# Performance work log

Hardware: AMD Instinct MI355X
Metric: run time of the kernel (lower is better)

## Reference

```python
import jax, jax.numpy as jnp
import numpy as np

VOCAB = 30000  # opts.numofingr
EPS = 1e-12


def setup_inputs() -> dict:
    key = jax.random.key(0)
    ks = jax.random.split(key, 8)
    B, L = 4096, 20
    ingrs = jax.random.randint(ks[0], (B, L), 0, VOCAB, dtype=jnp.int32)
    lengths = jax.random.randint(ks[1], (B,), 0, 21, dtype=jnp.int32)
    # MLP params: Linear(VOCAB,512) -> ReLU -> Linear(512,1024) -> ReLU -> Linear(1024,2047)
    # Stored so that one-hot @ W1 == W1[ingr]; i.e. W1 has shape [VOCAB, 512].
    W1 = jax.random.normal(ks[2], (VOCAB, 512), dtype=jnp.float32) * (1.0 / np.sqrt(VOCAB))
    b1 = jax.random.normal(ks[3], (512,), dtype=jnp.float32) * 0.01
    W2 = jax.random.normal(ks[4], (512, 1024), dtype=jnp.float32) * (1.0 / np.sqrt(512))
    b2 = jax.random.normal(ks[5], (1024,), dtype=jnp.float32) * 0.01
    W3 = jax.random.normal(ks[6], (1024, 2047), dtype=jnp.float32) * (1.0 / np.sqrt(1024))
    b3 = jax.random.normal(ks[7], (2047,), dtype=jnp.float32) * 0.01
    return {"ingrs": ingrs, "lengths": lengths,
            "W1": W1, "b1": b1, "W2": W2, "b2": b2, "W3": W3, "b3": b3}


def reference(ingrs, lengths, W1, b1, W2, b2, W3, b3):
    # One-hot x MLP first layer == embedding row gather: [B, L, 512]
    h1 = jax.nn.relu(W1[ingrs] + b1)
    h2 = jax.nn.relu(jnp.einsum('blh,hk->blk', h1, W2) + b2)   # [B, L, 1024]
    emb = jnp.einsum('blk,ko->blo', h2, W3) + b3               # [B, L, 2047]
    # L2-normalize each ingredient embedding (torch norm(p=2, dim=1) on [1,2047])
    nrm = jnp.sqrt(jnp.sum(emb * emb, axis=-1, keepdims=True))
    emb = emb / jnp.maximum(nrm, EPS)
    # Masked sum over valid ingredients (ingr_ln truncation in the source)
    L = ingrs.shape[1]
    mask = (jnp.arange(L)[None, :] < lengths[:, None]).astype(emb.dtype)  # [B, L]
    return jnp.einsum('blo,bl->bo', emb, mask)                 # [B, 2047]
```

## Files before the change

### kernel.cpp

```cpp
#include <hip/hip_runtime.h>

#define VOCAB 30000
#define MPAD  30080
#define MT_PAD 240

typedef __attribute__((ext_vector_type(8))) short bf16x8;
typedef __attribute__((ext_vector_type(4))) float f32x4;

__device__ __forceinline__ unsigned short f2bf(float f) {
    unsigned int u = __builtin_bit_cast(unsigned int, f);
    u += 0x7fffu + ((u >> 16) & 1u);
    return (unsigned short)(u >> 16);
}
__device__ __forceinline__ float bf2f(unsigned int h) {
    unsigned int u = h << 16;
    return __builtin_bit_cast(float, u);
}

__device__ __forceinline__ void async16(const void* g, void* l) {
    __builtin_amdgcn_global_load_lds(
        (__attribute__((address_space(1))) void*)g,
        (__attribute__((address_space(3))) void*)l, 16, 0, 0);
}

__global__ void k_mark(const int* __restrict__ ingrs, const int* __restrict__ lengths,
                       int* __restrict__ flags, int* __restrict__ cnt)
{
    const int i = blockIdx.x * 256 + threadIdx.x;
    if (i == 0) *cnt = 0;
    if (i >= 4096 * 20) return;
    const int b = i / 20;
    const int l = i - b * 20;
    if (l < lengths[b]) flags[ingrs[i]] = 1;
}

__global__ void k_assign(const int* __restrict__ flags, int* __restrict__ remap,
                         int* __restrict__ cnt)
{
    const int i = blockIdx.x * 256 + threadIdx.x;
    if (i < VOCAB && flags[i] == 1) remap[i] = atomicAdd(cnt, 1);
}


__device__ __forceinline__ void transpose_body(
    const float* __restrict__ in, unsigned short* __restrict__ out,
    int K, int Nin, int n0, int k0, int tid, float (*t)[65])
{
#pragma unroll
    for (int p = 0; p < 16; ++p) {
        const int lin = p * 256 + tid;
        const int kk = lin >> 6, nn = lin & 63;
        const int n = n0 + nn;
        t[kk][nn] = (n < Nin) ? in[(size_t)(k0 + kk) * Nin + n] : 0.f;
    }
    __syncthreads();
#pragma unroll
    for (int p = 0; p < 16; ++p) {
        const int lin = p * 256 + tid;
        const int nn = lin >> 6, kk = lin & 63;
        out[(size_t)(n0 + nn) * K + k0 + kk] = f2bf(t[kk][nn]);
    }
}

__device__ __forceinline__ void gemm_body(
    unsigned short* smem,
    const unsigned short* __restrict__ A, const unsigned short* __restrict__ BT,
    const float* __restrict__ bias, int bias_n, unsigned short* __restrict__ C,
    int K, int N, int relu, int mc, int id, int nt_shift)
{
    const int w  = id >> 3;
    const int n_tile = w & ((1 << nt_shift) - 1);
    const int m_tile = (id & 7) + ((w >> nt_shift) << 3);
    const int m0 = m_tile * 128;
    if (m0 >= mc) return;
    const int n0 = n_tile * 128;

    unsigned short* As = smem;
    unsigned short* Bs = smem + 8192;

    const int tid  = threadIdx.x;
    const int lane = tid & 63;
    const int wid  = tid >> 6;
    const int wr   = wid >> 1;
    const int wc   = wid & 1;
    const int q  = lane >> 4;
    const int ml = lane & 15;

    f32x4 acc[4][4];
    const f32x4 zero = {0.f, 0.f, 0.f, 0.f};
#pragma unroll
    for (int i = 0; i < 4; ++i)
#pragma unroll
        for (int j = 0; j < 4; ++j) acc[i][j] = zero;

    const int rg = lane >> 3;
    const int kc = (lane & 7) ^ rg;
    const unsigned short* pA = A  + (size_t)(m0 + wid * 32 + rg) * K + kc * 8;
    const unsigned short* pB = BT + (size_t)(n0 + wid * 32 + rg) * K + kc * 8;
    unsigned short* lA = &As[wid * 4 * 512 + lane * 8];
    unsigned short* lB = &Bs[wid * 4 * 512 + lane * 8];

    const int swz0 = (q ^ (ml & 7)) * 8;

    for (int k0 = 0; k0 < K; k0 += 64) {
#pragma unroll
        for (int gg = 0; gg < 4; ++gg) {
            async16(pA + (size_t)gg * 8 * K, lA + gg * 512);
            async16(pB + (size_t)gg * 8 * K, lB + gg * 512);
        }
        pA += 64; pB += 64;
        __syncthreads();

        bf16x8 af[4], bfr[4];
#pragma unroll
        for (int t = 0; t < 4; ++t) {
            af[t]  = *(const bf16x8*)&As[(wr * 64 + t * 16 + ml) * 64 + swz0];
            bfr[t] = *(const bf16x8*)&Bs[(wc * 64 + t * 16 + ml) * 64 + swz0];
        }
#pragma unroll
        for (int i = 0; i < 4; ++i)
#pragma unroll
            for (int j = 0; j < 4; ++j)
                acc[i][j] = __builtin_amdgcn_mfma_f32_16x16x32_bf16(
                    af[i], bfr[j], acc[i][j], 0, 0, 0);
#pragma unroll
        for (int t = 0; t < 4; ++t) {
            af[t]  = *(const bf16x8*)&As[(wr * 64 + t * 16 + ml) * 64 + (swz0 ^ 32)];
            bfr[t] = *(const bf16x8*)&Bs[(wc * 64 + t * 16 + ml) * 64 + (swz0 ^ 32)];
        }
#pragma unroll
        for (int i = 0; i < 4; ++i)
#pragma unroll
            for (int j = 0; j < 4; ++j)
                acc[i][j] = __builtin_amdgcn_mfma_f32_16x16x32_bf16(
                    af[i], bfr[j], acc[i][j], 0, 0, 0);

        __syncthreads();
    }

#pragma unroll
    for (int i = 0; i < 4; ++i) {
#pragma unroll
        for (int j = 0; j < 4; ++j) {
#pragma unroll
            for (int r = 0; r < 4; ++r) {
                const int rl = wr * 64 + i * 16 + q * 4 + r;
                const int cl = wc * 64 + j * 16 + ml;
                float v = acc[i][j][r];
                const int col = n0 + cl;
                v += (col < bias_n) ? bias[col] : 0.f;
                if (relu) v = fmaxf(v, 0.f);
                smem[rl * 136 + cl] = f2bf(v);
            }
        }
    }
    __syncthreads();
#pragma unroll
    for (int p = 0; p < 8; ++p) {
        const int rr = p * 16 + (tid >> 4);
        const int cc = tid & 15;
        const uint4 val = *(const uint4*)&smem[rr * 136 + cc * 8];
        *(uint4*)&C[(size_t)(m0 + rr) * N + n0 + cc * 8] = val;
    }
}

__global__ __launch_bounds__(256)
void k_prep(const float* __restrict__ W1, const float* __restrict__ b1,
            const int* __restrict__ flags, const int* __restrict__ remap,
            unsigned short* __restrict__ A1,
            const float* __restrict__ W2, unsigned short* __restrict__ W2T)
{
    __shared__ float t[64][65];
    const int bid = blockIdx.x;
    const int tid = threadIdx.x;

    if (bid < 15000) {
        const int id = bid * 2 + (tid >> 7);
        if (flags[id] != 1) return;
        const int row = remap[id];
        const int k4  = (tid & 127) * 4;
        const float4 w  = *(const float4*)(W1 + (size_t)id * 512 + k4);
        const float4 bb = *(const float4*)(b1 + k4);
        unsigned short o[4];
        o[0] = f2bf(fmaxf(w.x + bb.x, 0.f));
        o[1] = f2bf(fmaxf(w.y + bb.y, 0.f));
        o[2] = f2bf(fmaxf(w.z + bb.z, 0.f));
        o[3] = f2bf(fmaxf(w.w + bb.w, 0.f));
        *(uint2*)(A1 + (size_t)row * 512 + k4) = *(const uint2*)o;
    } else {
        const int local = bid - 15000;
        transpose_body(W2, W2T, 512, 1024, (local & 15) * 64, (local >> 4) * 64, tid, t);
    }
}

__global__ __launch_bounds__(256)
void k_gemm1(const unsigned short* __restrict__ A1, const unsigned short* __restrict__ W2T,
             const float* __restrict__ b2, unsigned short* __restrict__ H2,
             const int* __restrict__ cnt,
             const float* __restrict__ W3, unsigned short* __restrict__ W3T,
             const int* __restrict__ ingrs, const int* __restrict__ lengths,
             const int* __restrict__ remap, int* __restrict__ slots)
{
    __shared__ __align__(16) unsigned short smem[128 * 136];
    const int bid = blockIdx.x;
    if (bid < MT_PAD * 8) {
        const int mc = (*cnt + 127) & ~127;
        gemm_body(smem, A1, W2T, b2, 1024, H2, 512, 1024, 1, mc, bid, 3);
    } else if (bid < MT_PAD * 8 + 512) {
        const int local = bid - MT_PAD * 8;
        transpose_body(W3, W3T, 1024, 2047, (local & 31) * 64, (local >> 5) * 64,
                       threadIdx.x, (float(*)[65])smem);
    } else {
        const int i = (bid - (MT_PAD * 8 + 512)) * 256 + threadIdx.x;
        if (i < 4096 * 20) {
            const int b = i / 20;
            const int l = i - b * 20;
            if (l < lengths[b]) slots[i] = remap[ingrs[i]];
        }
    }
}

__global__ __launch_bounds__(256)
void k_gemm2(const unsigned short* __restrict__ H2, const unsigned short* __restrict__ W3T,
             const float* __restrict__ b3, unsigned short* __restrict__ Table,
             const int* __restrict__ cnt)
{
    __shared__ __align__(16) unsigned short smem[128 * 136];
    const int mc = (*cnt + 127) & ~127;
    gemm_body(smem, H2, W3T, b3, 2047, Table, 1024, 2048, 0, mc, blockIdx.x, 4);
}

__global__ __launch_bounds__(64)
void k_gather(const int* __restrict__ lengths, const int* __restrict__ slots,
              const unsigned short* __restrict__ Table, float* __restrict__ out)
{
    const int b    = blockIdx.x;
    const int lane = threadIdx.x;

    float acc[32];
#pragma unroll
    for (int j = 0; j < 32; ++j) acc[j] = 0.f;

    const int len = lengths[b];
    if (len > 0) {
        uint4 u[4];
        {
            const int slot = slots[b * 20];
            const uint4* rp = (const uint4*)(Table + (size_t)slot * 2048);
#pragma unroll
            for (int c = 0; c < 4; ++c) u[c] = rp[c * 64 + lane];
        }
        for (int l = 0; l < len; ++l) {
            uint4 cu[4];
#pragma unroll
            for (int c = 0; c < 4; ++c) cu[c] = u[c];
            if (l + 1 < len) {
                const int ns = slots[b * 20 + l + 1];
                const uint4* rp = (const uint4*)(Table + (size_t)ns * 2048);
#pragma unroll
                for (int c = 0; c < 4; ++c) u[c] = rp[c * 64 + lane];
            }
            float v[32];
#pragma unroll
            for (int c = 0; c < 4; ++c) {
                v[c*8+0] = bf2f(cu[c].x & 0xffffu); v[c*8+1] = bf2f(cu[c].x >> 16);
                v[c*8+2] = bf2f(cu[c].y & 0xffffu); v[c*8+3] = bf2f(cu[c].y >> 16);
                v[c*8+4] = bf2f(cu[c].z & 0xffffu); v[c*8+5] = bf2f(cu[c].z >> 16);
                v[c*8+6] = bf2f(cu[c].w & 0xffffu); v[c*8+7] = bf2f(cu[c].w >> 16);
            }
            float s = 0.f;
#pragma unroll
            for (int j = 0; j < 32; ++j) s += v[j] * v[j];
#pragma unroll
            for (int off = 1; off < 64; off <<= 1) s += __shfl_xor(s, off, 64);
            const float invn = 1.0f / fmaxf(sqrtf(s), 1e-12f);
#pragma unroll
            for (int j = 0; j < 32; ++j) acc[j] += v[j] * invn;
        }
    }

    const size_t base = (size_t)b * 2047;
#pragma unroll
    for (int c = 0; c < 4; ++c) {
        const int col = (c * 64 + lane) * 8;
#pragma unroll
        for (int j = 0; j < 8; ++j)
            if (col + j < 2047) out[base + col + j] = acc[c * 8 + j];
    }
}


extern "C" void kernel_launch(void* const* d_in, const int* in_sizes, int n_in,
                              void* d_out, int out_size, void* d_ws, size_t ws_size,
                              hipStream_t stream)
{
    const int*   ingrs   = (const int*)d_in[0];
    const int*   lengths = (const int*)d_in[1];
    const float* W1 = (const float*)d_in[2];
    const float* b1 = (const float*)d_in[3];
    const float* W2 = (const float*)d_in[4];
    const float* b2 = (const float*)d_in[5];
    const float* W3 = (const float*)d_in[6];
    const float* b3 = (const float*)d_in[7];
    float* out = (float*)d_out;

    char* ws = (char*)d_ws;
    unsigned short* A1    = (unsigned short*)(ws);
    unsigned short* H2    = (unsigned short*)(ws + 30801920);
    unsigned short* Table = (unsigned short*)(ws + 92405760);
    unsigned short* W2T   = (unsigned short*)(ws + 215613440);
    unsigned short* W3T   = (unsigned short*)(ws + 216662016);
    int*            flags = (int*)(ws + 220856320);
    int*            remap = (int*)(ws + 220976320);
    int*            cnt   = (int*)(ws + 221096320);
    int*            slots = (int*)(ws + 221216448);

    k_mark  <<<(4096 * 20 + 255) / 256, 256, 0, stream>>>(ingrs, lengths, flags, cnt);
    k_assign<<<(VOCAB + 255) / 256, 256, 0, stream>>>(flags, remap, cnt);
    k_prep<<<15128, 256, 0, stream>>>(W1, b1, flags, remap, A1, W2, W2T);
    k_gemm1<<<MT_PAD * 8 + 512 + 320, 256, 0, stream>>>(
        A1, W2T, b2, H2, cnt, W3, W3T, ingrs, lengths, remap, slots);
    k_gemm2<<<MT_PAD * 16, 256, 0, stream>>>(H2, W3T, b3, Table, cnt);

    k_gather<<<4096, 64, 0, stream>>>(lengths, slots, Table, out);
}
```

Before: 328.3 us.

## Switch GEMMs to 256x256 tiles with double-buffered async LDS pipeline

Replaces the 128x128 single-buffered GEMM body with a 256x256 tile, 512-thread, double-buffered kernel that prefetches the next K-slices while issuing MFMAs, with barrier/priority scheduling. The W3 transpose and slot computation move into the prep kernel, so the GEMM kernels run only GEMM work. The gather kernel prefetches two rows ahead and uses vectorized float4 output stores. Larger tiles raise data reuse and cut global traffic, but 128KB of LDS per block and higher register pressure limit occupancy, and padding to 256 rows wastes more compute.

```diff
diff --git a/kernel.cpp b/kernel.cpp
--- a/kernel.cpp
+++ b/kernel.cpp
@@ -2,7 +2,7 @@
 
 #define VOCAB 30000
 #define MPAD  30080
-#define MT_PAD 240
+#define G_MT  120
 
 typedef __attribute__((ext_vector_type(8))) short bf16x8;
 typedef __attribute__((ext_vector_type(4))) float f32x4;
@@ -41,7 +41,6 @@
     if (i < VOCAB && flags[i] == 1) remap[i] = atomicAdd(cnt, 1);
 }
 
-
 __device__ __forceinline__ void transpose_body(
     const float* __restrict__ in, unsigned short* __restrict__ out,
     int K, int Nin, int n0, int k0, int tid, float (*t)[65])
@@ -62,105 +61,149 @@
     }
 }
 
-__device__ __forceinline__ void gemm_body(
-    unsigned short* smem,
+#define MF(a, b, c) __builtin_amdgcn_mfma_f32_16x16x32_bf16(a, b, c, 0, 0, 0)
+
+#define G_U(AB, H, B_, T) do {                                                 \
+        const unsigned short* _s = ((AB) ? gB : gA)                            \
+            + (size_t)((H) * 128) * K + (size_t)(T) * 64;                      \
+        unsigned short* _d = &lds[(AB) * 32768 + (B_) * 16384                  \
+            + ((H) * 128) * 64 + dst0];                                        \
+        async16(_s, _d);                                                       \
+        async16(_s + (size_t)8 * K, _d + 8 * 64);                              \
+    } while (0)
+
+#define LDA(I, S) (*(const bf16x8*)&lds[cb + ((wr * 128 + (I) * 16 + ml) * 64) + ((((S) * 4 + q) ^ m7) * 8)])
+#define LDB(J, S) (*(const bf16x8*)&lds[32768 + cb + ((wc * 64 + (J) * 16 + ml) * 64) + ((((S) * 4 + q) ^ m7) * 8)])
+
+#define G_MFMA16(AI0, BF)                                                      \
+        _Pragma("unroll")                                                      \
+        for (int i = 0; i < 4; ++i)                                            \
+        _Pragma("unroll")                                                      \
+        for (int j = 0; j < 4; ++j)                                            \
+            acc[(AI0) + i][j] = MF(afr[i], BF[j], acc[(AI0) + i][j]);
+
+#define G_BAR()  __builtin_amdgcn_s_barrier()
+#define G_LGKM() do { asm volatile("s_waitcnt lgkmcnt(0)" ::: "memory");       \
+                      __builtin_amdgcn_sched_barrier(0); } while (0)
+
+__device__ __forceinline__ void gemm256_body(
+    unsigned short* lds,
     const unsigned short* __restrict__ A, const unsigned short* __restrict__ BT,
     const float* __restrict__ bias, int bias_n, unsigned short* __restrict__ C,
-    int K, int N, int relu, int mc, int id, int nt_shift)
+    int K, int NK, int N, int relu, int mc, int id, int nt_shift)
 {
     const int w  = id >> 3;
     const int n_tile = w & ((1 << nt_shift) - 1);
     const int m_tile = (id & 7) + ((w >> nt_shift) << 3);
-    const int m0 = m_tile * 128;
+    const int m0 = m_tile * 256;
     if (m0 >= mc) return;
-    const int n0 = n_tile * 128;
-
-    unsigned short* As = smem;
-    unsigned short* Bs = smem + 8192;
+    const int n0 = n_tile * 256;
 
     const int tid  = threadIdx.x;
     const int lane = tid & 63;
-    const int wid  = tid >> 6;
-    const int wr   = wid >> 1;
-    const int wc   = wid & 1;
-    const int q  = lane >> 4;
-    const int ml = lane & 15;
-
-    f32x4 acc[4][4];
+    const int w0   = tid >> 6;
+    const int wr   = w0 >> 2;
+    const int wc   = w0 & 3;
+    const int q    = lane >> 4;
+    const int ml   = lane & 15;
+    const int m7   = ml & 7;
+
+    f32x4 acc[8][4];
     const f32x4 zero = {0.f, 0.f, 0.f, 0.f};
 #pragma unroll
-    for (int i = 0; i < 4; ++i)
+    for (int i = 0; i < 8; ++i)
 #pragma unroll
         for (int j = 0; j < 4; ++j) acc[i][j] = zero;
 
     const int rg = lane >> 3;
     const int kc = (lane & 7) ^ rg;
-    const unsigned short* pA = A  + (size_t)(m0 + wid * 32 + rg) * K + kc * 8;
-    const unsigned short* pB = BT + (size_t)(n0 + wid * 32 + rg) * K + kc * 8;
-    unsigned short* lA = &As[wid * 4 * 512 + lane * 8];
-    unsigned short* lB = &Bs[wid * 4 * 512 + lane * 8];
-
-    const int swz0 = (q ^ (ml & 7)) * 8;
-
-    for (int k0 = 0; k0 < K; k0 += 64) {
-#pragma unroll
-        for (int gg = 0; gg < 4; ++gg) {
-            async16(pA + (size_t)gg * 8 * K, lA + gg * 512);
-            async16(pB + (size_t)gg * 8 * K, lB + gg * 512);
-        }
-        pA += 64; pB += 64;
+    const unsigned short* gA = A  + (size_t)(m0 + w0 * 16 + rg) * K + kc * 8;
+    const unsigned short* gB = BT + (size_t)(n0 + w0 * 16 + rg) * K + kc * 8;
+    const int dst0 = (w0 * 16) * 64 + lane * 8;
+
+    G_U(0, 0, 0, 0); G_U(0, 1, 0, 0); G_U(1, 0, 0, 0); G_U(1, 1, 0, 0);
+    G_U(0, 0, 1, 1); G_U(1, 0, 1, 1);
+    asm volatile("s_waitcnt vmcnt(4)" ::: "memory");
+    G_BAR();
+
+    for (int t = 0; t < NK; ++t) {
+        const int cb  = (t & 1) * 16384;
+        const int nxt = (t & 1) ^ 1;
+        bf16x8 afr[4], bS0[4], bS1[4];
+
+#pragma unroll
+        for (int j = 0; j < 4; ++j) bS0[j] = LDB(j, 0);
+#pragma unroll
+        for (int i = 0; i < 4; ++i) afr[i] = LDA(i, 0);
+        if (t + 1 < NK) G_U(0, 1, nxt, t + 1);
+        G_BAR(); G_LGKM();
+        __builtin_amdgcn_s_setprio(1);
+        G_MFMA16(0, bS0)
+        __builtin_amdgcn_s_setprio(0);
+        G_BAR();
+
+#pragma unroll
+        for (int i = 0; i < 4; ++i) afr[i] = LDA(4 + i, 0);
+        if (t + 1 < NK) G_U(1, 1, nxt, t + 1);
+        G_BAR(); G_LGKM();
+        __builtin_amdgcn_s_setprio(1);
+        G_MFMA16(4, bS0)
+        __builtin_amdgcn_s_setprio(0);
+        G_BAR();
+
+#pragma unroll
+        for (int j = 0; j < 4; ++j) bS1[j] = LDB(j, 1);
+#pragma unroll
+        for (int i = 0; i < 4; ++i) afr[i] = LDA(i, 1);
+        G_BAR(); G_LGKM();
+        __builtin_amdgcn_s_setprio(1);
+        G_MFMA16(0, bS1)
+        __builtin_amdgcn_s_setprio(0);
+        G_BAR();
+
+#pragma unroll
+        for (int i = 0; i < 4; ++i) afr[i] = LDA(4 + i, 1);
+        if (t + 2 < NK) { G_U(0, 0, t & 1, t + 2); G_U(1, 0, t & 1, t + 2); }
+        G_BAR(); G_LGKM();
+        __builtin_amdgcn_s_setprio(1);
+        G_MFMA16(4, bS1)
+        __builtin_amdgcn_s_setprio(0);
+        if (t + 2 < NK) asm volatile("s_waitcnt vmcnt(4)" ::: "memory");
+        else            asm volatile("s_waitcnt vmcnt(0)" ::: "memory");
+        G_BAR();
+    }
+
+    float bv[4];
+#pragma unroll
+    for (int j = 0; j < 4; ++j) {
+        const int col = n0 + wc * 64 + j * 16 + ml;
+        bv[j] = (col < bias_n) ? bias[col] : 0.f;
+    }
+    for (int h = 0; h < 2; ++h) {
+        if (wr == h) {
+#pragma unroll
+            for (int i = 0; i < 8; ++i)
+#pragma unroll
+                for (int j = 0; j < 4; ++j)
+#pragma unroll
+                    for (int r = 0; r < 4; ++r) {
+                        float v = acc[i][j][r] + bv[j];
+                        if (relu) v = fmaxf(v, 0.f);
+                        lds[(i * 16 + q * 4 + r) * 280 + wc * 64 + j * 16 + ml] = f2bf(v);
+                    }
+        }
         __syncthreads();
-
-        bf16x8 af[4], bfr[4];
-#pragma unroll
-        for (int t = 0; t < 4; ++t) {
-            af[t]  = *(const bf16x8*)&As[(wr * 64 + t * 16 + ml) * 64 + swz0];
-            bfr[t] = *(const bf16x8*)&Bs[(wc * 64 + t * 16 + ml) * 64 + swz0];
-        }
-#pragma unroll
-        for (int i = 0; i < 4; ++i)
-#pragma unroll
-            for (int j = 0; j < 4; ++j)
-                acc[i][j] = __builtin_amdgcn_mfma_f32_16x16x32_bf16(
-                    af[i], bfr[j], acc[i][j], 0, 0, 0);
-#pragma unroll
-        for (int t = 0; t < 4; ++t) {
-            af[t]  = *(const bf16x8*)&As[(wr * 64 + t * 16 + ml) * 64 + (swz0 ^ 32)];
-            bfr[t] = *(const bf16x8*)&Bs[(wc * 64 + t * 16 + ml) * 64 + (swz0 ^ 32)];
-        }
-#pragma unroll
-        for (int i = 0; i < 4; ++i)
-#pragma unroll
-            for (int j = 0; j < 4; ++j)
-                acc[i][j] = __builtin_amdgcn_mfma_f32_16x16x32_bf16(
-                    af[i], bfr[j], acc[i][j], 0, 0, 0);
-
+#pragma unroll
+        for (int p = 0; p < 8; ++p) {
+            const int row  = p * 16 + (tid >> 5);
+            const int c8   = (tid & 31) * 8;
+            const int grow = m0 + h * 128 + row;
+            if (grow < MPAD) {
+                *(uint4*)&C[(size_t)grow * N + n0 + c8] =
+                    *(const uint4*)&lds[row * 280 + c8];
+            }
+        }
         __syncthreads();
-    }
-
-#pragma unroll
-    for (int i = 0; i < 4; ++i) {
-#pragma unroll
-        for (int j = 0; j < 4; ++j) {
-#pragma unroll
-            for (int r = 0; r < 4; ++r) {
-                const int rl = wr * 64 + i * 16 + q * 4 + r;
-                const int cl = wc * 64 + j * 16 + ml;
-                float v = acc[i][j][r];
-                const int col = n0 + cl;
-                v += (col < bias_n) ? bias[col] : 0.f;
-                if (relu) v = fmaxf(v, 0.f);
-                smem[rl * 136 + cl] = f2bf(v);
-            }
-        }
-    }
-    __syncthreads();
-#pragma unroll
-    for (int p = 0; p < 8; ++p) {
-        const int rr = p * 16 + (tid >> 4);
-        const int cc = tid & 15;
-        const uint4 val = *(const uint4*)&smem[rr * 136 + cc * 8];
-        *(uint4*)&C[(size_t)(m0 + rr) * N + n0 + cc * 8] = val;
     }
 }
 
@@ -168,7 +211,10 @@
 void k_prep(const float* __restrict__ W1, const float* __restrict__ b1,
             const int* __restrict__ flags, const int* __restrict__ remap,
             unsigned short* __restrict__ A1,
-            const float* __restrict__ W2, unsigned short* __restrict__ W2T)
+            const float* __restrict__ W2, unsigned short* __restrict__ W2T,
+            const float* __restrict__ W3, unsigned short* __restrict__ W3T,
+            const int* __restrict__ ingrs, const int* __restrict__ lengths,
+            int* __restrict__ slots)
 {
     __shared__ float t[64][65];
     const int bid = blockIdx.x;
@@ -187,31 +233,14 @@
         o[2] = f2bf(fmaxf(w.z + bb.z, 0.f));
         o[3] = f2bf(fmaxf(w.w + bb.w, 0.f));
         *(uint2*)(A1 + (size_t)row * 512 + k4) = *(const uint2*)o;
-    } else {
+    } else if (bid < 15128) {
         const int local = bid - 15000;
         transpose_body(W2, W2T, 512, 1024, (local & 15) * 64, (local >> 4) * 64, tid, t);
-    }
-}
-
-__global__ __launch_bounds__(256)
-void k_gemm1(const unsigned short* __restrict__ A1, const unsigned short* __restrict__ W2T,
-             const float* __restrict__ b2, unsigned short* __restrict__ H2,
-             const int* __restrict__ cnt,
-             const float* __restrict__ W3, unsigned short* __restrict__ W3T,
-             const int* __restrict__ ingrs, const int* __restrict__ lengths,
-             const int* __restrict__ remap, int* __restrict__ slots)
-{
-    __shared__ __align__(16) unsigned short smem[128 * 136];
-    const int bid = blockIdx.x;
-    if (bid < MT_PAD * 8) {
-        const int mc = (*cnt + 127) & ~127;
-        gemm_body(smem, A1, W2T, b2, 1024, H2, 512, 1024, 1, mc, bid, 3);
-    } else if (bid < MT_PAD * 8 + 512) {
-        const int local = bid - MT_PAD * 8;
-        transpose_body(W3, W3T, 1024, 2047, (local & 31) * 64, (local >> 5) * 64,
-                       threadIdx.x, (float(*)[65])smem);
+    } else if (bid < 15640) {
+        const int local = bid - 15128;
+        transpose_body(W3, W3T, 1024, 2047, (local & 31) * 64, (local >> 5) * 64, tid, t);
     } else {
-        const int i = (bid - (MT_PAD * 8 + 512)) * 256 + threadIdx.x;
+        const int i = (bid - 15640) * 256 + tid;
         if (i < 4096 * 20) {
             const int b = i / 20;
             const int l = i - b * 20;
@@ -220,14 +249,24 @@
     }
 }
 
-__global__ __launch_bounds__(256)
+__global__ __launch_bounds__(512, 2)
+void k_gemm1(const unsigned short* __restrict__ A1, const unsigned short* __restrict__ W2T,
+             const float* __restrict__ b2, unsigned short* __restrict__ H2,
+             const int* __restrict__ cnt)
+{
+    __shared__ __align__(16) unsigned short lds[65536];
+    const int mc = (*cnt + 255) & ~255;
+    gemm256_body(lds, A1, W2T, b2, 1024, H2, 512, 8, 1024, 1, mc, blockIdx.x, 2);
+}
+
+__global__ __launch_bounds__(512, 2)
 void k_gemm2(const unsigned short* __restrict__ H2, const unsigned short* __restrict__ W3T,
              const float* __restrict__ b3, unsigned short* __restrict__ Table,
              const int* __restrict__ cnt)
 {
-    __shared__ __align__(16) unsigned short smem[128 * 136];
-    const int mc = (*cnt + 127) & ~127;
-    gemm_body(smem, H2, W3T, b3, 2047, Table, 1024, 2048, 0, mc, blockIdx.x, 4);
+    __shared__ __align__(16) unsigned short lds[65536];
+    const int mc = (*cnt + 255) & ~255;
+    gemm256_body(lds, H2, W3T, b3, 2047, Table, 1024, 16, 2048, 0, mc, blockIdx.x, 3);
 }
 
 __global__ __launch_bounds__(64)
@@ -243,22 +282,25 @@
 
     const int len = lengths[b];
     if (len > 0) {
-        uint4 u[4];
+        uint4 u0[4], u1[4];
         {
-            const int slot = slots[b * 20];
-            const uint4* rp = (const uint4*)(Table + (size_t)slot * 2048);
-#pragma unroll
-            for (int c = 0; c < 4; ++c) u[c] = rp[c * 64 + lane];
+            const uint4* rp = (const uint4*)(Table + (size_t)slots[b * 20] * 2048);
+#pragma unroll
+            for (int c = 0; c < 4; ++c) u0[c] = rp[c * 64 + lane];
+        }
+        if (len > 1) {
+            const uint4* rp = (const uint4*)(Table + (size_t)slots[b * 20 + 1] * 2048);
+#pragma unroll
+            for (int c = 0; c < 4; ++c) u1[c] = rp[c * 64 + lane];
         }
         for (int l = 0; l < len; ++l) {
             uint4 cu[4];
 #pragma unroll
-            for (int c = 0; c < 4; ++c) cu[c] = u[c];
-            if (l + 1 < len) {
-                const int ns = slots[b * 20 + l + 1];
-                const uint4* rp = (const uint4*)(Table + (size_t)ns * 2048);
-#pragma unroll
-                for (int c = 0; c < 4; ++c) u[c] = rp[c * 64 + lane];
+            for (int c = 0; c < 4; ++c) { cu[c] = u0[c]; u0[c] = u1[c]; }
+            if (l + 2 < len) {
+                const uint4* rp = (const uint4*)(Table + (size_t)slots[b * 20 + l + 2] * 2048);
+#pragma unroll
+                for (int c = 0; c < 4; ++c) u1[c] = rp[c * 64 + lane];
             }
             float v[32];
 #pragma unroll
@@ -283,9 +325,13 @@
 #pragma unroll
     for (int c = 0; c < 4; ++c) {
         const int col = (c * 64 + lane) * 8;
-#pragma unroll
-        for (int j = 0; j < 8; ++j)
-            if (col + j < 2047) out[base + col + j] = acc[c * 8 + j];
+        if (c < 3 || lane != 63) {
+            *(float4*)&out[base + col]     = *(const float4*)&acc[c * 8];
+            *(float4*)&out[base + col + 4] = *(const float4*)&acc[c * 8 + 4];
+        } else {
+#pragma unroll
+            for (int j = 0; j < 7; ++j) out[base + col + j] = acc[c * 8 + j];
+        }
     }
 }
 
@@ -317,10 +363,10 @@
 
     k_mark  <<<(4096 * 20 + 255) / 256, 256, 0, stream>>>(ingrs, lengths, flags, cnt);
     k_assign<<<(VOCAB + 255) / 256, 256, 0, stream>>>(flags, remap, cnt);
-    k_prep<<<15128, 256, 0, stream>>>(W1, b1, flags, remap, A1, W2, W2T);
-    k_gemm1<<<MT_PAD * 8 + 512 + 320, 256, 0, stream>>>(
-        A1, W2T, b2, H2, cnt, W3, W3T, ingrs, lengths, remap, slots);
-    k_gemm2<<<MT_PAD * 16, 256, 0, stream>>>(H2, W3T, b3, Table, cnt);
+    k_prep<<<15960, 256, 0, stream>>>(W1, b1, flags, remap, A1, W2, W2T,
+                                      W3, W3T, ingrs, lengths, slots);
+    k_gemm1<<<G_MT * 4, 512, 0, stream>>>(A1, W2T, b2, H2, cnt);
+    k_gemm2<<<G_MT * 8, 512, 0, stream>>>(H2, W3T, b3, Table, cnt);
 
     k_gather<<<4096, 64, 0, stream>>>(lengths, slots, Table, out);
 }
```

After: 309.3 us. -5.8%, faster.
